# Performance work log

Hardware: AMD Instinct MI355X
Metric: run time of the kernel (lower is better)

The kernel has to match this reference:

```python
import jax, jax.numpy as jnp
import numpy as np

N_NODES = 50000
N_EDGES = 800000
N_GRAPHS = 128
D_IN = 64
D_H = 64
D_OUT = 16
N_GIN_LAYERS = 4  # num_layers - 1
BN_EPS = 1e-5


def setup_inputs() -> dict:
    key = jax.random.key(0)
    ks = jax.random.split(key, 12)
    s = 0.05  # weight scale for numerical sanity
    x = jax.random.normal(ks[0], (N_NODES, D_IN), dtype=jnp.float32)
    w = jax.random.uniform(ks[1], (N_EDGES,), dtype=jnp.float32)
    src = jax.random.randint(ks[2], (N_EDGES,), 0, N_NODES, dtype=jnp.int32)
    dst = jax.random.randint(ks[3], (N_EDGES,), 0, N_NODES, dtype=jnp.int32)
    graph_ids = jnp.sort(jax.random.randint(ks[4], (N_NODES,), 0, N_GRAPHS, dtype=jnp.int32))
    eps = jnp.zeros((N_GIN_LAYERS,), dtype=jnp.float32)
    mlp_W1 = jax.random.normal(ks[5], (N_GIN_LAYERS, D_IN, D_H), dtype=jnp.float32) * s
    mlp_b1 = jnp.zeros((N_GIN_LAYERS, D_H), dtype=jnp.float32)
    mlp_bn_g = jnp.ones((N_GIN_LAYERS, D_H), dtype=jnp.float32)
    mlp_bn_b = jnp.zeros((N_GIN_LAYERS, D_H), dtype=jnp.float32)
    mlp_W2 = jax.random.normal(ks[6], (N_GIN_LAYERS, D_H, D_H), dtype=jnp.float32) * s
    mlp_b2 = jnp.zeros((N_GIN_LAYERS, D_H), dtype=jnp.float32)
    bn_g = jnp.ones((N_GIN_LAYERS, D_H), dtype=jnp.float32)
    bn_b = jnp.zeros((N_GIN_LAYERS, D_H), dtype=jnp.float32)
    pred_W = jax.random.normal(ks[7], (N_GIN_LAYERS + 1, D_H, D_OUT), dtype=jnp.float32) * s
    pred_b = jnp.zeros((N_GIN_LAYERS + 1, D_OUT), dtype=jnp.float32)
    return {"x": x, "w": w, "src": src, "dst": dst, "graph_ids": graph_ids,
            "eps": eps, "mlp_W1": mlp_W1, "mlp_b1": mlp_b1,
            "mlp_bn_g": mlp_bn_g, "mlp_bn_b": mlp_bn_b,
            "mlp_W2": mlp_W2, "mlp_b2": mlp_b2,
            "bn_g": bn_g, "bn_b": bn_b, "pred_W": pred_W, "pred_b": pred_b}


def _batchnorm(h, gamma, beta):
    # training-mode BatchNorm1d: normalize by batch mean / biased variance
    mu = jnp.mean(h, axis=0)
    var = jnp.mean((h - mu) ** 2, axis=0)
    return gamma * (h - mu) * jax.lax.rsqrt(var + BN_EPS) + beta


def reference(x, w, src, dst, graph_ids, eps, mlp_W1, mlp_b1, mlp_bn_g, mlp_bn_b,
              mlp_W2, mlp_b2, bn_g, bn_b, pred_W, pred_b):
    def pool(h):  # graph readout: sum over nodes of each graph -> [G, D]
        return jax.ops.segment_sum(h, graph_ids, num_segments=N_GRAPHS)

    h = x
    # layer-0 prediction on raw features (dropout p=0 -> identity)
    score = pool(h) @ pred_W[0] + pred_b[0]
    for l in range(N_GIN_LAYERS):
        # message: edge weight * source feature, reduce: sum over in-edges
        msg = w[:, None] * h[src]                                  # [E, D]
        h_neigh = jax.ops.segment_sum(msg, dst, num_segments=N_NODES)
        h = (1.0 + eps[l]) * h + h_neigh                           # eps self-aggregate
        # 2-layer MLP: Linear -> BN -> ReLU -> Linear
        t = _batchnorm(h @ mlp_W1[l] + mlp_b1[l], mlp_bn_g[l], mlp_bn_b[l])
        h = jax.nn.relu(t) @ mlp_W2[l] + mlp_b2[l]
        # outer BN + ReLU
        h = jax.nn.relu(_batchnorm(h, bn_g[l], bn_b[l]))
        score = score + pool(h) @ pred_W[l + 1] + pred_b[l + 1]
    return score
```

## Files before the change

### kernel.cpp

```cpp
#include <hip/hip_runtime.h>
#include <hip/hip_bf16.h>

#define N_NODES 50000
#define N_EDGES 800000
#define N_GRAPHS 128
#define NB2 391
#define BCAP 4096
#define EPB 4096
#define PART_BLOCKS ((N_EDGES + EPB - 1) / EPB)
#define NSLOT 32

typedef __attribute__((ext_vector_type(8))) short short8;
typedef __attribute__((ext_vector_type(4))) float f32x4;

union B16x8 { uint4 u; short8 s; };

__device__ __forceinline__ unsigned bf16rn(float f) {
    unsigned u = __float_as_uint(f);
    return (u + 0x7FFFu + ((u >> 16) & 1u)) >> 16;
}
__device__ __forceinline__ unsigned packbf2(float a, float b) {
    return bf16rn(a) | (bf16rn(b) << 16);
}
__device__ __forceinline__ float2 unpkbf2(unsigned v) {
    return make_float2(__uint_as_float(v << 16), __uint_as_float(v & 0xFFFF0000u));
}

__device__ __forceinline__ void bn_coef_from_slots(const float* __restrict__ stats,
                                                   const float* __restrict__ gamma,
                                                   const float* __restrict__ beta, int n, int t,
                                                   float* sc, float* sh) {
    float su = 0.f, sq = 0.f;
#pragma unroll 8
    for (int s5 = 0; s5 < NSLOT; ++s5) {
        su += stats[s5 * 128 + t];
        sq += stats[s5 * 128 + 64 + t];
    }
    float inv_n = 1.0f / (float)n;
    float mean = su * inv_n;
    float var = sq * inv_n - mean * mean;
    float s = gamma[t] * rsqrtf(var + 1e-5f);
    sc[t] = s;
    sh[t] = beta[t] - mean * s;
}


__global__ __launch_bounds__(256) void setup_partition_kernel(
    const int* __restrict__ dst, const int* __restrict__ src, const float* __restrict__ w,
    int* __restrict__ cursor, int2* __restrict__ tmp, int E,
    const float* __restrict__ x, unsigned* __restrict__ xb,
    const float* __restrict__ W1, const float* __restrict__ W2,
    unsigned short* __restrict__ Wt, const int* __restrict__ gid,
    int* __restrict__ start, int n, int ngraphs) {
    __shared__ int lh[NB2];
    __shared__ int lbase[NB2];
    const int t = threadIdx.x;

    const int gtid = blockIdx.x * 256 + t;
    const int gsz = gridDim.x * 256;
    for (int i = gtid; i < n * 8; i += gsz) {
        float4 a = *(const float4*)(x + (size_t)i * 8);
        float4 b = *(const float4*)(x + (size_t)i * 8 + 4);
        uint4 o;
        o.x = packbf2(a.x, a.y);
        o.y = packbf2(a.z, a.w);
        o.z = packbf2(b.x, b.y);
        o.w = packbf2(b.z, b.w);
        *(uint4*)(xb + (size_t)i * 4) = o;
    }
    for (int i = gtid; i < 8 * 4096; i += gsz) {
        int mat = i >> 12, k = (i >> 6) & 63, nn = i & 63, l = mat >> 1;
        const float* Wsrc = (mat & 1) ? (W2 + l * 4096) : (W1 + l * 4096);
        Wt[(size_t)mat * 4096 + nn * 64 + k] = (unsigned short)bf16rn(Wsrc[k * 64 + nn]);
    }
    for (int i = gtid; i < n; i += gsz) {
        int g = gid[i];
        if (i == 0) {
            for (int q = 0; q <= g; ++q) start[q] = 0;
        } else {
            int p = gid[i - 1];
            if (p != g)
                for (int q = p + 1; q <= g; ++q) start[q] = i;
        }
        if (i == n - 1)
            for (int q = g + 1; q <= ngraphs; ++q) start[q] = n;
    }

    for (int i = t; i < NB2; i += 256) lh[i] = 0;
    __syncthreads();
    int base = blockIdx.x * EPB;
    int d[EPB / 256];
#pragma unroll
    for (int i = 0; i < EPB / 256; ++i) {
        int e = base + i * 256 + t;
        d[i] = (e < E) ? dst[e] : -1;
        if (d[i] >= 0) atomicAdd(&lh[d[i] >> 7], 1);
    }
    __syncthreads();
    for (int i = t; i < NB2; i += 256) {
        int v = lh[i];
        if (v) lbase[i] = atomicAdd(&cursor[i], v);
        lh[i] = 0;
    }
    __syncthreads();
#pragma unroll
    for (int i = 0; i < EPB / 256; ++i) {
        int e = base + i * 256 + t;
        if (d[i] >= 0) {
            int b = d[i] >> 7;
            int dl = d[i] & 127;
            int rank = atomicAdd(&lh[b], 1);
            tmp[(size_t)b * BCAP + lbase[b] + rank] =
                make_int2(src[e] | (dl << 16), __float_as_int(w[e]));
        }
    }
}


__global__ __launch_bounds__(256) void node_sort_kernel(const int2* __restrict__ tmp,
                                                        const int* __restrict__ ecnt,
                                                        int2* __restrict__ row_se,
                                                        unsigned* __restrict__ pack, int n) {
    __shared__ int hist[128];
    __shared__ int run[128];
    __shared__ int s[256];
    const int t = threadIdx.x;
    const int b = blockIdx.x;
    int cnt = ecnt[b];
    if (cnt > BCAP) cnt = BCAP;
    const int2* tb2 = tmp + (size_t)b * BCAP;
    const int gbase = b * BCAP;

    if (t < 128) hist[t] = 0;
    __syncthreads();
    for (int j = t; j < cnt; j += 256) atomicAdd(&hist[(tb2[j].x >> 16) & 127], 1);
    __syncthreads();
    int v = (t < 128) ? hist[t] : 0;
    s[t] = v;
    __syncthreads();
    for (int off = 1; off < 128; off <<= 1) {
        int u = (t >= off) ? s[t - off] : 0;
        __syncthreads();
        s[t] += u;
        __syncthreads();
    }
    if (t < 128) {
        int excl = s[t] - v;
        int node = b * 128 + t;
        if (node < n) row_se[node] = make_int2(gbase + excl, gbase + excl + v);
        run[t] = gbase + excl;
    }
    __syncthreads();
    for (int j = t; j < cnt; j += 256) {
        int2 p = tb2[j];
        int pos = atomicAdd(&run[(p.x >> 16) & 127], 1);
        pack[pos] = (unsigned)(p.x & 0xFFFF) | (bf16rn(__int_as_float(p.y)) << 16);
    }
}


__global__ __launch_bounds__(256) void agg_kernel(const unsigned* __restrict__ hb,
                                                  const unsigned* __restrict__ pack,
                                                  const int2* __restrict__ row_se,
                                                  const float* __restrict__ eps, int layer,
                                                  unsigned* __restrict__ outb, int n,
                                                  const float* __restrict__ stats,
                                                  const float* __restrict__ gamma,
                                                  const float* __restrict__ beta,
                                                  int transform, int agg_blocks,
                                                  const int* __restrict__ start,
                                                  const float* __restrict__ pW,
                                                  const float* __restrict__ pb,
                                                  float* __restrict__ score) {
    __shared__ float sc[64], sh[64];
    const int t = threadIdx.x;
    if (transform) {
        if (t < 64) bn_coef_from_slots(stats, gamma, beta, n, t, sc, sh);
        __syncthreads();
    }

    if ((int)blockIdx.x >= agg_blocks) {
        __shared__ float red[16][68];
        __shared__ float pl[64];
        const int g = blockIdx.x - agg_blocks;
        const int r16 = t >> 4;
        const int qq = t & 15;
        const int k0 = qq << 2;
        int i0 = start[g], i1 = start[g + 1];
        float4 ps = make_float4(0.f, 0.f, 0.f, 0.f);
        for (int i = i0 + r16; i < i1; i += 16) {
            uint2 u = *(const uint2*)(hb + (size_t)i * 32 + qq * 2);
            float2 a = unpkbf2(u.x);
            float2 b = unpkbf2(u.y);
            if (transform) {
                a.x = fmaxf(fmaf(a.x, sc[k0 + 0], sh[k0 + 0]), 0.f);
                a.y = fmaxf(fmaf(a.y, sc[k0 + 1], sh[k0 + 1]), 0.f);
                b.x = fmaxf(fmaf(b.x, sc[k0 + 2], sh[k0 + 2]), 0.f);
                b.y = fmaxf(fmaf(b.y, sc[k0 + 3], sh[k0 + 3]), 0.f);
            }
            ps.x += a.x; ps.y += a.y; ps.z += b.x; ps.w += b.y;
        }
        red[r16][k0 + 0] = ps.x;
        red[r16][k0 + 1] = ps.y;
        red[r16][k0 + 2] = ps.z;
        red[r16][k0 + 3] = ps.w;
        __syncthreads();
        if (t < 64) {
            float s = 0.f;
#pragma unroll
            for (int r = 0; r < 16; ++r) s += red[r][t];
            pl[t] = s;
        }
        __syncthreads();
        if (t < 16) {
            float s = pb[t];
#pragma unroll 8
            for (int d = 0; d < 64; ++d) s += pl[d] * pW[d * 16 + t];
            score[g * 16 + t] = transform ? (score[g * 16 + t] + s) : s;
        }
        return;
    }

    int node = blockIdx.x * 4 + (t >> 6);
    if (node >= n) return;
    const int lane = t & 63;
    const int slot = lane >> 4;
    const int li = lane & 15;

    float4 sc4 = make_float4(1.f, 1.f, 1.f, 1.f);
    float4 sh4 = make_float4(0.f, 0.f, 0.f, 0.f);
    if (transform) {
        sc4 = *(const float4*)(sc + li * 4);
        sh4 = *(const float4*)(sh + li * 4);
    }
    float e1 = 1.0f + eps[layer];

    float4 acc = make_float4(0.f, 0.f, 0.f, 0.f);
    {
        uint2 su = *(const uint2*)(hb + (size_t)node * 32 + li * 2);
        if (slot == 0) {
            float2 a = unpkbf2(su.x), b = unpkbf2(su.y);
            if (transform) {
                a.x = fmaxf(fmaf(a.x, sc4.x, sh4.x), 0.f);
                a.y = fmaxf(fmaf(a.y, sc4.y, sh4.y), 0.f);
                b.x = fmaxf(fmaf(b.x, sc4.z, sh4.z), 0.f);
                b.y = fmaxf(fmaf(b.y, sc4.w, sh4.w), 0.f);
            }
            acc.x = e1 * a.x; acc.y = e1 * a.y; acc.z = e1 * b.x; acc.w = e1 * b.y;
        }
    }

    int2 se = row_se[node];
    int j0 = se.x, j1 = se.y;
    int j = j0;
    unsigned pk[4];
    if (j < j1) {
#pragma unroll
        for (int u = 0; u < 4; ++u) {
            int idx = j + slot + u * 4;
            pk[u] = pack[idx < j1 ? idx : j1 - 1];
        }
    }
    while (j < j1) {
        float wv[4];
        uint2 g[4];
#pragma unroll
        for (int u = 0; u < 4; ++u) {
            int jj = j + slot + u * 4;
            wv[u] = (jj < j1) ? __uint_as_float(pk[u] & 0xFFFF0000u) : 0.f;
        }
#pragma unroll
        for (int u = 0; u < 4; ++u)
            g[u] = *(const uint2*)(hb + (size_t)(pk[u] & 0xFFFFu) * 32 + li * 2);
        j += 16;
        if (j < j1) {
#pragma unroll
            for (int u = 0; u < 4; ++u) {
                int idx = j + slot + u * 4;
                pk[u] = pack[idx < j1 ? idx : j1 - 1];
            }
        }
#pragma unroll
        for (int u = 0; u < 4; ++u) {
            float2 a = unpkbf2(g[u].x), b = unpkbf2(g[u].y);
            if (transform) {
                a.x = fmaxf(fmaf(a.x, sc4.x, sh4.x), 0.f);
                a.y = fmaxf(fmaf(a.y, sc4.y, sh4.y), 0.f);
                b.x = fmaxf(fmaf(b.x, sc4.z, sh4.z), 0.f);
                b.y = fmaxf(fmaf(b.y, sc4.w, sh4.w), 0.f);
            }
            acc.x += wv[u] * a.x;
            acc.y += wv[u] * a.y;
            acc.z += wv[u] * b.x;
            acc.w += wv[u] * b.y;
        }
    }

    acc.x += __shfl_xor(acc.x, 16);
    acc.y += __shfl_xor(acc.y, 16);
    acc.z += __shfl_xor(acc.z, 16);
    acc.w += __shfl_xor(acc.w, 16);
    acc.x += __shfl_xor(acc.x, 32);
    acc.y += __shfl_xor(acc.y, 32);
    acc.z += __shfl_xor(acc.z, 32);
    acc.w += __shfl_xor(acc.w, 32);
    if (slot == 0) {
        uint2 o;
        o.x = packbf2(acc.x, acc.y);
        o.y = packbf2(acc.z, acc.w);
        *(uint2*)(outb + (size_t)node * 32 + li * 2) = o;
    }
}


#define GTILE 128

__global__ __launch_bounds__(256) void mfma_gemm(const unsigned short* __restrict__ A,
                                                 const unsigned short* __restrict__ Wt,
                                                 const float* __restrict__ bias,
                                                 unsigned short* __restrict__ out,
                                                 float* __restrict__ stats_out,
                                                 const float* __restrict__ stats_in,
                                                 const float* __restrict__ gamma,
                                                 const float* __restrict__ beta,
                                                 int n, int transform) {
    __shared__ float sc[64], sh[64];
    __shared__ unsigned short cstage[GTILE * 64];
    __shared__ float rsum[64 * 17];
    __shared__ float rsq[64 * 17];

    const int t = threadIdx.x;
    const int wid = t >> 6;
    const int lane = t & 63;
    const int m = lane & 15;
    const int q = lane >> 4;
    const int rowbase = blockIdx.x * GTILE + wid * 32;

    B16x8 af[2][2];
#pragma unroll
    for (int tr = 0; tr < 2; ++tr) {
        int gr = rowbase + tr * 16 + m;
#pragma unroll
        for (int kc = 0; kc < 2; ++kc) {
            if (gr < n)
                af[tr][kc].u = *(const uint4*)(A + (size_t)gr * 64 + kc * 32 + q * 8);
            else
                af[tr][kc].u = make_uint4(0, 0, 0, 0);
        }
    }

    B16x8 bf[4][2];
#pragma unroll
    for (int tc = 0; tc < 4; ++tc)
#pragma unroll
        for (int kc = 0; kc < 2; ++kc)
            bf[tc][kc].u = *(const uint4*)(Wt + (size_t)(tc * 16 + m) * 64 + kc * 32 + q * 8);

    if (transform && t < 64) bn_coef_from_slots(stats_in, gamma, beta, n, t, sc, sh);
    __syncthreads();

    if (transform) {
        int k0base = q * 8;
#pragma unroll
        for (int tr = 0; tr < 2; ++tr)
#pragma unroll
            for (int kc = 0; kc < 2; ++kc) {
                int k0 = kc * 32 + k0base;
                float4 s0 = *(const float4*)(sc + k0);
                float4 s1 = *(const float4*)(sc + k0 + 4);
                float4 h0 = *(const float4*)(sh + k0);
                float4 h1 = *(const float4*)(sh + k0 + 4);
                uint4 uu = af[tr][kc].u;
                float2 p0 = unpkbf2(uu.x), p1 = unpkbf2(uu.y);
                float2 p2 = unpkbf2(uu.z), p3 = unpkbf2(uu.w);
                p0.x = fmaxf(fmaf(p0.x, s0.x, h0.x), 0.f);
                p0.y = fmaxf(fmaf(p0.y, s0.y, h0.y), 0.f);
                p1.x = fmaxf(fmaf(p1.x, s0.z, h0.z), 0.f);
                p1.y = fmaxf(fmaf(p1.y, s0.w, h0.w), 0.f);
                p2.x = fmaxf(fmaf(p2.x, s1.x, h1.x), 0.f);
                p2.y = fmaxf(fmaf(p2.y, s1.y, h1.y), 0.f);
                p3.x = fmaxf(fmaf(p3.x, s1.z, h1.z), 0.f);
                p3.y = fmaxf(fmaf(p3.y, s1.w, h1.w), 0.f);
                uu.x = packbf2(p0.x, p0.y);
                uu.y = packbf2(p1.x, p1.y);
                uu.z = packbf2(p2.x, p2.y);
                uu.w = packbf2(p3.x, p3.y);
                af[tr][kc].u = uu;
            }
    }

    f32x4 acc[2][4];
#pragma unroll
    for (int tr = 0; tr < 2; ++tr)
#pragma unroll
        for (int tc = 0; tc < 4; ++tc) {
            acc[tr][tc] = (f32x4){0.f, 0.f, 0.f, 0.f};
            acc[tr][tc] = __builtin_amdgcn_mfma_f32_16x16x32_bf16(af[tr][0].s, bf[tc][0].s,
                                                                  acc[tr][tc], 0, 0, 0);
            acc[tr][tc] = __builtin_amdgcn_mfma_f32_16x16x32_bf16(af[tr][1].s, bf[tc][1].s,
                                                                  acc[tr][tc], 0, 0, 0);
        }

    float bc[4];
#pragma unroll
    for (int tc = 0; tc < 4; ++tc) bc[tc] = bias[tc * 16 + m];

    float psum[4] = {0, 0, 0, 0}, psq[4] = {0, 0, 0, 0};
#pragma unroll
    for (int tr = 0; tr < 2; ++tr)
#pragma unroll
        for (int reg = 0; reg < 4; ++reg) {
            int rl = wid * 32 + tr * 16 + q * 4 + reg;
            int gr = blockIdx.x * GTILE + rl;
            int sw = ((rl >> 2) & 3) << 4;
            bool ok = gr < n;
#pragma unroll
            for (int tc = 0; tc < 4; ++tc) {
                float val = acc[tr][tc][reg] + bc[tc];
                int col = tc * 16 + m;
                cstage[rl * 64 + (col ^ sw)] = (unsigned short)bf16rn(ok ? val : 0.f);
                if (ok) {
                    psum[tc] += val;
                    psq[tc] += val * val;
                }
            }
        }

    int contrib = wid * 4 + q;
#pragma unroll
    for (int tc = 0; tc < 4; ++tc) {
        int c = tc * 16 + m;
        rsum[c * 17 + contrib] = psum[tc];
        rsq[c * 17 + contrib] = psq[tc];
    }
    __syncthreads();

#pragma unroll
    for (int rep = 0; rep < 4; ++rep) {
        int idx = rep * 256 + t;
        int rl = idx >> 3;
        int k = idx & 7;
        int gr = blockIdx.x * GTILE + rl;
        if (gr < n) {
            int klds = k ^ (((rl >> 2) & 3) << 1);
            uint4 v = *(const uint4*)(cstage + rl * 64 + klds * 8);
            *(uint4*)(out + (size_t)gr * 64 + k * 8) = v;
        }
    }

    if (t < 64) {
        float s = 0.f, qq = 0.f;
#pragma unroll
        for (int i = 0; i < 16; ++i) {
            s += rsum[t * 17 + i];
            qq += rsq[t * 17 + i];
        }
        int slot = (blockIdx.x & (NSLOT - 1)) * 128;
        atomicAdd(&stats_out[slot + t], s);
        atomicAdd(&stats_out[slot + 64 + t], qq);
    }
}


__global__ __launch_bounds__(256) void pool_score_kernel(const unsigned* __restrict__ hb,
                                                         const int* __restrict__ start,
                                                         const float* __restrict__ pW,
                                                         const float* __restrict__ pb,
                                                         float* __restrict__ score,
                                                         const float* __restrict__ stats,
                                                         const float* __restrict__ gamma,
                                                         const float* __restrict__ beta,
                                                         int n, int mode) {
    __shared__ float red[16][68];
    __shared__ float sc[64], sh[64], pl[64];
    const int t = threadIdx.x;
    const int g = blockIdx.x;
    if (mode && t < 64) bn_coef_from_slots(stats, gamma, beta, n, t, sc, sh);
    __syncthreads();

    const int r16 = t >> 4;
    const int qq = t & 15;
    const int k0 = qq << 2;
    int i0 = start[g], i1 = start[g + 1];
    float4 ps = make_float4(0.f, 0.f, 0.f, 0.f);
    for (int i = i0 + r16; i < i1; i += 16) {
        uint2 u = *(const uint2*)(hb + (size_t)i * 32 + qq * 2);
        float2 a = unpkbf2(u.x);
        float2 b = unpkbf2(u.y);
        if (mode) {
            a.x = fmaxf(fmaf(a.x, sc[k0 + 0], sh[k0 + 0]), 0.f);
            a.y = fmaxf(fmaf(a.y, sc[k0 + 1], sh[k0 + 1]), 0.f);
            b.x = fmaxf(fmaf(b.x, sc[k0 + 2], sh[k0 + 2]), 0.f);
            b.y = fmaxf(fmaf(b.y, sc[k0 + 3], sh[k0 + 3]), 0.f);
        }
        ps.x += a.x; ps.y += a.y; ps.z += b.x; ps.w += b.y;
    }
    red[r16][k0 + 0] = ps.x;
    red[r16][k0 + 1] = ps.y;
    red[r16][k0 + 2] = ps.z;
    red[r16][k0 + 3] = ps.w;
    __syncthreads();
    if (t < 64) {
        float s = 0.f;
#pragma unroll
        for (int r = 0; r < 16; ++r) s += red[r][t];
        pl[t] = s;
    }
    __syncthreads();
    if (t < 16) {
        float s = pb[t];
#pragma unroll 8
        for (int d = 0; d < 64; ++d) s += pl[d] * pW[d * 16 + t];
        score[g * 16 + t] = mode ? (score[g * 16 + t] + s) : s;
    }
}


extern "C" void kernel_launch(void* const* d_in, const int* in_sizes, int n_in,
                              void* d_out, int out_size, void* d_ws, size_t ws_size,
                              hipStream_t stream) {
    const float* x = (const float*)d_in[0];
    const float* w = (const float*)d_in[1];
    const int* src = (const int*)d_in[2];
    const int* dst = (const int*)d_in[3];
    const int* gid = (const int*)d_in[4];
    const float* eps = (const float*)d_in[5];
    const float* W1 = (const float*)d_in[6];
    const float* b1 = (const float*)d_in[7];
    const float* bng = (const float*)d_in[8];
    const float* bnb = (const float*)d_in[9];
    const float* W2 = (const float*)d_in[10];
    const float* b2 = (const float*)d_in[11];
    const float* og = (const float*)d_in[12];
    const float* ob = (const float*)d_in[13];
    const float* pW = (const float*)d_in[14];
    const float* pb = (const float*)d_in[15];
    float* out = (float*)d_out;

    const int N = N_NODES, E = N_EDGES, G = N_GRAPHS;
    const int SETSZ = NSLOT * 128;

    unsigned* base = (unsigned*)d_ws;
    unsigned* xb = base;
    unsigned* HA = xb + (size_t)N * 32;
    unsigned* HB = HA + (size_t)N * 32;
    float* stats = (float*)(HB + (size_t)N * 32);
    int* cursor = (int*)(stats + 8 * SETSZ);
    int* start = cursor + NB2 + 1;
    int2* row_se = (int2*)(start + 132);
    unsigned short* Wt = (unsigned short*)(row_se + N + 8);
    int2* tmp = (int2*)(Wt + 8 * 4096);
    unsigned* pack = (unsigned*)(tmp + (size_t)NB2 * BCAP);

    hipMemsetAsync(stats, 0, (size_t)(8 * SETSZ + NB2 + 1) * sizeof(float), stream);

    hipLaunchKernelGGL(setup_partition_kernel, dim3(PART_BLOCKS), dim3(256), 0, stream, dst, src,
                       w, cursor, tmp, E, x, xb, W1, W2, Wt, gid, start, N, G);
    hipLaunchKernelGGL(node_sort_kernel, dim3(NB2), dim3(256), 0, stream, tmp, cursor, row_se,
                       pack, N);

    const int agg_blocks = (N + 3) / 4;
    const int gemm_blocks = (N + GTILE - 1) / GTILE;
    unsigned* cur = xb;
    unsigned* P = HA;
    unsigned* Q = HB;
    for (int l = 0; l < 4; ++l) {
        const float* tr_stats = (l == 0) ? nullptr : stats + (size_t)(2 * (l - 1) + 1) * SETSZ;
        const float* tr_g = (l == 0) ? nullptr : og + (l - 1) * 64;
        const float* tr_b = (l == 0) ? nullptr : ob + (l - 1) * 64;
        hipLaunchKernelGGL(agg_kernel, dim3(agg_blocks + G), dim3(256), 0, stream, cur, pack,
                           row_se, eps, l, P, N, tr_stats, tr_g, tr_b, l == 0 ? 0 : 1,
                           agg_blocks, start, pW + (size_t)l * 1024, pb + l * 16, out);
        hipLaunchKernelGGL(mfma_gemm, dim3(gemm_blocks), dim3(256), 0, stream,
                           (const unsigned short*)P, Wt + (size_t)(l * 2) * 4096, b1 + l * 64,
                           (unsigned short*)Q, stats + (size_t)(2 * l) * SETSZ,
                           (const float*)nullptr, (const float*)nullptr, (const float*)nullptr,
                           N, 0);
        hipLaunchKernelGGL(mfma_gemm, dim3(gemm_blocks), dim3(256), 0, stream,
                           (const unsigned short*)Q, Wt + (size_t)(l * 2 + 1) * 4096, b2 + l * 64,
                           (unsigned short*)P, stats + (size_t)(2 * l + 1) * SETSZ,
                           stats + (size_t)(2 * l) * SETSZ, bng + l * 64, bnb + l * 64, N, 1);
        cur = P;
        unsigned* t2 = P;
        P = Q;
        Q = t2;
    }
    hipLaunchKernelGGL(pool_score_kernel, dim3(G), dim3(256), 0, stream, cur, start,
                       pW + 4 * 1024, pb + 4 * 16, out, stats + (size_t)7 * SETSZ, og + 3 * 64,
                       ob + 3 * 64, N, 1);
}
```

Measured before the change: 369.0 us.

## Fuse first MLP GEMM into aggregation kernel with per-block MFMA epilogue

Aggregation blocks now handle 8 nodes with 512 threads, stage the aggregated rows in shared memory, and have one wavefront run the first 64x64 linear layer with bf16 MFMA. That wavefront writes the bf16 result and accumulates BN statistics into 128 atomic slots. This removes one GEMM launch and the round trip of the aggregated features through global memory. In exchange only one of eight wavefronts does the GEMM, half the MFMA rows are padding, and more atomic slots must be reduced.

```diff
diff --git a/kernel.cpp b/kernel.cpp
--- a/kernel.cpp
+++ b/kernel.cpp
@@ -9,6 +9,9 @@
 #define EPB 4096
 #define PART_BLOCKS ((N_EDGES + EPB - 1) / EPB)
 #define NSLOT 32
+#define NSLOTA 128
+#define AGG_NPB 8
+#define AGG_BLOCKS (N_NODES / AGG_NPB)
 
 typedef __attribute__((ext_vector_type(8))) short short8;
 typedef __attribute__((ext_vector_type(4))) float f32x4;
@@ -29,10 +32,10 @@
 __device__ __forceinline__ void bn_coef_from_slots(const float* __restrict__ stats,
                                                    const float* __restrict__ gamma,
                                                    const float* __restrict__ beta, int n, int t,
-                                                   float* sc, float* sh) {
+                                                   float* sc, float* sh, int nslot) {
     float su = 0.f, sq = 0.f;
 #pragma unroll 8
-    for (int s5 = 0; s5 < NSLOT; ++s5) {
+    for (int s5 = 0; s5 < nslot; ++s5) {
         su += stats[s5 * 128 + t];
         sq += stats[s5 * 128 + 64 + t];
     }
@@ -159,36 +162,35 @@
 }
 
 
-__global__ __launch_bounds__(256) void agg_kernel(const unsigned* __restrict__ hb,
-                                                  const unsigned* __restrict__ pack,
-                                                  const int2* __restrict__ row_se,
-                                                  const float* __restrict__ eps, int layer,
-                                                  unsigned* __restrict__ outb, int n,
-                                                  const float* __restrict__ stats,
-                                                  const float* __restrict__ gamma,
-                                                  const float* __restrict__ beta,
-                                                  int transform, int agg_blocks,
-                                                  const int* __restrict__ start,
-                                                  const float* __restrict__ pW,
-                                                  const float* __restrict__ pb,
-                                                  float* __restrict__ score) {
+__global__ __launch_bounds__(512) void agg_gemm1_kernel(
+    const unsigned* __restrict__ hb, const unsigned* __restrict__ pack,
+    const int2* __restrict__ row_se, const float* __restrict__ eps, int layer,
+    unsigned short* __restrict__ Qo, int n,
+    const float* __restrict__ stats, const float* __restrict__ gamma,
+    const float* __restrict__ beta, int transform,
+    const int* __restrict__ start, const float* __restrict__ pW,
+    const float* __restrict__ pb, float* __restrict__ score,
+    const unsigned short* __restrict__ Wt1, const float* __restrict__ b1,
+    float* __restrict__ s1) {
     __shared__ float sc[64], sh[64];
+    __shared__ float st[16 * 68];
+    __shared__ unsigned short cstage[8 * 72];
     const int t = threadIdx.x;
     if (transform) {
-        if (t < 64) bn_coef_from_slots(stats, gamma, beta, n, t, sc, sh);
+        if (t < 64) bn_coef_from_slots(stats, gamma, beta, n, t, sc, sh, NSLOT);
         __syncthreads();
     }
 
-    if ((int)blockIdx.x >= agg_blocks) {
-        __shared__ float red[16][68];
+    if ((int)blockIdx.x >= AGG_BLOCKS) {
+        __shared__ float red[32][68];
         __shared__ float pl[64];
-        const int g = blockIdx.x - agg_blocks;
+        const int g = blockIdx.x - AGG_BLOCKS;
         const int r16 = t >> 4;
         const int qq = t & 15;
         const int k0 = qq << 2;
         int i0 = start[g], i1 = start[g + 1];
         float4 ps = make_float4(0.f, 0.f, 0.f, 0.f);
-        for (int i = i0 + r16; i < i1; i += 16) {
+        for (int i = i0 + r16; i < i1; i += 32) {
             uint2 u = *(const uint2*)(hb + (size_t)i * 32 + qq * 2);
             float2 a = unpkbf2(u.x);
             float2 b = unpkbf2(u.y);
@@ -208,7 +210,7 @@
         if (t < 64) {
             float s = 0.f;
 #pragma unroll
-            for (int r = 0; r < 16; ++r) s += red[r][t];
+            for (int r = 0; r < 32; ++r) s += red[r][t];
             pl[t] = s;
         }
         __syncthreads();
@@ -221,9 +223,9 @@
         return;
     }
 
-    int node = blockIdx.x * 4 + (t >> 6);
-    if (node >= n) return;
+    const int wid = t >> 6;
     const int lane = t & 63;
+    const int node = blockIdx.x * AGG_NPB + wid;
     const int slot = lane >> 4;
     const int li = lane & 15;
 
@@ -304,11 +306,72 @@
     acc.y += __shfl_xor(acc.y, 32);
     acc.z += __shfl_xor(acc.z, 32);
     acc.w += __shfl_xor(acc.w, 32);
-    if (slot == 0) {
-        uint2 o;
-        o.x = packbf2(acc.x, acc.y);
-        o.y = packbf2(acc.z, acc.w);
-        *(uint2*)(outb + (size_t)node * 32 + li * 2) = o;
+    if (slot == 0) *(float4*)(st + wid * 68 + li * 4) = acc;
+    __syncthreads();
+
+    if (wid != 0) return;
+    const int m = lane & 15;
+    const int q = lane >> 4;
+
+    B16x8 af[2];
+#pragma unroll
+    for (int kc = 0; kc < 2; ++kc) {
+        const float* sp = st + m * 68 + kc * 32 + q * 8;
+        float4 fa = *(const float4*)sp;
+        float4 fb = *(const float4*)(sp + 4);
+        af[kc].u = make_uint4(packbf2(fa.x, fa.y), packbf2(fa.z, fa.w),
+                              packbf2(fb.x, fb.y), packbf2(fb.z, fb.w));
+    }
+
+    f32x4 acc1[4];
+#pragma unroll
+    for (int tc = 0; tc < 4; ++tc) {
+        B16x8 bf0, bf1;
+        bf0.u = *(const uint4*)(Wt1 + (size_t)(tc * 16 + m) * 64 + q * 8);
+        bf1.u = *(const uint4*)(Wt1 + (size_t)(tc * 16 + m) * 64 + 32 + q * 8);
+        acc1[tc] = (f32x4){0.f, 0.f, 0.f, 0.f};
+        acc1[tc] = __builtin_amdgcn_mfma_f32_16x16x32_bf16(af[0].s, bf0.s, acc1[tc], 0, 0, 0);
+        acc1[tc] = __builtin_amdgcn_mfma_f32_16x16x32_bf16(af[1].s, bf1.s, acc1[tc], 0, 0, 0);
+    }
+
+    float bc[4];
+#pragma unroll
+    for (int tc = 0; tc < 4; ++tc) bc[tc] = b1[tc * 16 + m];
+
+    float psum[4] = {0, 0, 0, 0}, psq[4] = {0, 0, 0, 0};
+#pragma unroll
+    for (int tc = 0; tc < 4; ++tc)
+#pragma unroll
+        for (int reg = 0; reg < 4; ++reg) {
+            int row = q * 4 + reg;
+            if (q < 2) {
+                float val = acc1[tc][reg] + bc[tc];
+                cstage[row * 72 + tc * 16 + m] = (unsigned short)bf16rn(val);
+                psum[tc] += val;
+                psq[tc] += val * val;
+            }
+        }
+#pragma unroll
+    for (int tc = 0; tc < 4; ++tc) {
+        psum[tc] += __shfl_xor(psum[tc], 16);
+        psum[tc] += __shfl_xor(psum[tc], 32);
+        psq[tc] += __shfl_xor(psq[tc], 16);
+        psq[tc] += __shfl_xor(psq[tc], 32);
+    }
+    if (lane < 16) {
+        int sl = (blockIdx.x & (NSLOTA - 1)) * 128;
+#pragma unroll
+        for (int tc = 0; tc < 4; ++tc) {
+            atomicAdd(&s1[sl + tc * 16 + lane], psum[tc]);
+            atomicAdd(&s1[sl + 64 + tc * 16 + lane], psq[tc]);
+        }
+    }
+
+    {
+        int row = lane >> 3;
+        int k = lane & 7;
+        uint4 v = *(const uint4*)(cstage + row * 72 + k * 8);
+        *(uint4*)(Qo + (size_t)(blockIdx.x * AGG_NPB + row) * 64 + k * 8) = v;
     }
 }
 
@@ -356,7 +419,7 @@
         for (int kc = 0; kc < 2; ++kc)
             bf[tc][kc].u = *(const uint4*)(Wt + (size_t)(tc * 16 + m) * 64 + kc * 32 + q * 8);
 
-    if (transform && t < 64) bn_coef_from_slots(stats_in, gamma, beta, n, t, sc, sh);
+    if (transform && t < 64) bn_coef_from_slots(stats_in, gamma, beta, n, t, sc, sh, NSLOTA);
     __syncthreads();
 
     if (transform) {
@@ -475,7 +538,7 @@
     __shared__ float sc[64], sh[64], pl[64];
     const int t = threadIdx.x;
     const int g = blockIdx.x;
-    if (mode && t < 64) bn_coef_from_slots(stats, gamma, beta, n, t, sc, sh);
+    if (mode && t < 64) bn_coef_from_slots(stats, gamma, beta, n, t, sc, sh, NSLOT);
     __syncthreads();
 
     const int r16 = t >> 4;
@@ -538,54 +601,49 @@
     float* out = (float*)d_out;
 
     const int N = N_NODES, E = N_EDGES, G = N_GRAPHS;
-    const int SETSZ = NSLOT * 128;
+    const int S1SZ = NSLOTA * 128;
+    const int S2SZ = NSLOT * 128;
 
     unsigned* base = (unsigned*)d_ws;
     unsigned* xb = base;
     unsigned* HA = xb + (size_t)N * 32;
     unsigned* HB = HA + (size_t)N * 32;
-    float* stats = (float*)(HB + (size_t)N * 32);
-    int* cursor = (int*)(stats + 8 * SETSZ);
+    unsigned* Qb = HB + (size_t)N * 32;
+    float* s1 = (float*)(Qb + (size_t)N * 32);
+    float* s2 = s1 + 4 * S1SZ;
+    int* cursor = (int*)(s2 + 4 * S2SZ);
     int* start = cursor + NB2 + 1;
     int2* row_se = (int2*)(start + 132);
     unsigned short* Wt = (unsigned short*)(row_se + N + 8);
     int2* tmp = (int2*)(Wt + 8 * 4096);
     unsigned* pack = (unsigned*)(tmp + (size_t)NB2 * BCAP);
 
-    hipMemsetAsync(stats, 0, (size_t)(8 * SETSZ + NB2 + 1) * sizeof(float), stream);
+    hipMemsetAsync(s1, 0, (size_t)(4 * S1SZ + 4 * S2SZ + NB2 + 1) * sizeof(float), stream);
 
     hipLaunchKernelGGL(setup_partition_kernel, dim3(PART_BLOCKS), dim3(256), 0, stream, dst, src,
                        w, cursor, tmp, E, x, xb, W1, W2, Wt, gid, start, N, G);
     hipLaunchKernelGGL(node_sort_kernel, dim3(NB2), dim3(256), 0, stream, tmp, cursor, row_se,
                        pack, N);
 
-    const int agg_blocks = (N + 3) / 4;
     const int gemm_blocks = (N + GTILE - 1) / GTILE;
     unsigned* cur = xb;
-    unsigned* P = HA;
-    unsigned* Q = HB;
+    unsigned* bufs[2] = {HA, HB};
     for (int l = 0; l < 4; ++l) {
-        const float* tr_stats = (l == 0) ? nullptr : stats + (size_t)(2 * (l - 1) + 1) * SETSZ;
+        const float* tr_stats = (l == 0) ? nullptr : s2 + (size_t)(l - 1) * S2SZ;
         const float* tr_g = (l == 0) ? nullptr : og + (l - 1) * 64;
         const float* tr_b = (l == 0) ? nullptr : ob + (l - 1) * 64;
-        hipLaunchKernelGGL(agg_kernel, dim3(agg_blocks + G), dim3(256), 0, stream, cur, pack,
-                           row_se, eps, l, P, N, tr_stats, tr_g, tr_b, l == 0 ? 0 : 1,
-                           agg_blocks, start, pW + (size_t)l * 1024, pb + l * 16, out);
+        unsigned* hn = bufs[l & 1];
+        hipLaunchKernelGGL(agg_gemm1_kernel, dim3(AGG_BLOCKS + G), dim3(512), 0, stream, cur,
+                           pack, row_se, eps, l, (unsigned short*)Qb, N, tr_stats, tr_g, tr_b,
+                           l == 0 ? 0 : 1, start, pW + (size_t)l * 1024, pb + l * 16, out,
+                           Wt + (size_t)(l * 2) * 4096, b1 + l * 64, s1 + (size_t)l * S1SZ);
         hipLaunchKernelGGL(mfma_gemm, dim3(gemm_blocks), dim3(256), 0, stream,
-                           (const unsigned short*)P, Wt + (size_t)(l * 2) * 4096, b1 + l * 64,
-                           (unsigned short*)Q, stats + (size_t)(2 * l) * SETSZ,
-                           (const float*)nullptr, (const float*)nullptr, (const float*)nullptr,
-                           N, 0);
-        hipLaunchKernelGGL(mfma_gemm, dim3(gemm_blocks), dim3(256), 0, stream,
-                           (const unsigned short*)Q, Wt + (size_t)(l * 2 + 1) * 4096, b2 + l * 64,
-                           (unsigned short*)P, stats + (size_t)(2 * l + 1) * SETSZ,
-                           stats + (size_t)(2 * l) * SETSZ, bng + l * 64, bnb + l * 64, N, 1);
-        cur = P;
-        unsigned* t2 = P;
-        P = Q;
-        Q = t2;
+                           (const unsigned short*)Qb, Wt + (size_t)(l * 2 + 1) * 4096,
+                           b2 + l * 64, (unsigned short*)hn, s2 + (size_t)l * S2SZ,
+                           s1 + (size_t)l * S1SZ, bng + l * 64, bnb + l * 64, N, 1);
+        cur = hn;
     }
     hipLaunchKernelGGL(pool_score_kernel, dim3(G), dim3(256), 0, stream, cur, start,
-                       pW + 4 * 1024, pb + 4 * 16, out, stats + (size_t)7 * SETSZ, og + 3 * 64,
+                       pW + 4 * 1024, pb + 4 * 16, out, s2 + (size_t)3 * S2SZ, og + 3 * 64,
                        ob + 3 * 64, N, 1);
 }
```

Measured after the change: 355.9 us. 1.04x faster.
